# Optimization experiments

Measured on AMD Instinct MI355X. Metric: run time of the kernel, lower is better.

Reference implementation:

```python
import jax, jax.numpy as jnp
import numpy as np

B, D, FD, HW, NH, NC = 8, 384, 256, 64, 8, 4
NP = HW * HW
HD = D // NH


def _ln(x, g, b, eps=1e-5):
    m = jnp.mean(x, -1, keepdims=True)
    v = jnp.mean((x - m) ** 2, -1, keepdims=True)
    return (x - m) / jnp.sqrt(v + eps) * g + b


def _grn(x, g, b, eps=1e-6):
    # x: [B, D, H, W]; global L2 norm per channel over spatial dims
    gx = jnp.sqrt(jnp.sum(x * x, axis=(-2, -1), keepdims=True))  # [B,D,1,1]
    nx = gx / (jnp.mean(gx, axis=-3, keepdims=True) + eps)
    return (1.0 + g[:, None, None]) * (x * nx) + b[:, None, None] + x


def _adaln(x, film, W, bW, g, b):
    gb = film @ W.T + bW                       # [B, 2D]
    gamma, beta = jnp.split(gb, 2, axis=-1)
    return _grn(x, g, b) * (1.0 + gamma)[:, :, None, None] + beta[:, :, None, None]


def setup_inputs() -> dict:
    ks = jax.random.split(jax.random.key(0), 24)
    n = lambda k, s: jax.random.normal(k, s, jnp.float32)
    w = lambda k, o, i: n(k, (o, i)) * 0.02
    return {
        "image": n(ks[0], (B, D, HW, HW)),
        "film_vector": n(ks[1], (B, FD)),
        "perm": jax.random.permutation(ks[2], NP).astype(jnp.int32),
        "Wq": w(ks[3], D, D), "bq": jnp.zeros(D),
        "Wk": w(ks[4], D, D), "bk": jnp.zeros(D),
        "Wv": w(ks[5], D, D), "bv": jnp.zeros(D),
        "Wo": w(ks[6], D, D), "bo": jnp.zeros(D),
        "lnq_g": jnp.ones(D), "lnq_b": jnp.zeros(D),
        "lnk_g": jnp.ones(D), "lnk_b": jnp.zeros(D),
        "ada1_W": n(ks[7], (2 * D, FD)) * 0.001, "ada1_b": jnp.zeros(2 * D),
        "grn1_g": jnp.zeros(D), "grn1_b": jnp.zeros(D),
        "ada2_W": n(ks[8], (2 * D, FD)) * 0.001, "ada2_b": jnp.zeros(2 * D),
        "grn2_g": jnp.zeros(D), "grn2_b": jnp.zeros(D),
        "conv1_W": w(ks[9], 4 * D, D), "conv1_b": jnp.zeros(4 * D),
        "conv2_W": w(ks[10], D, 4 * D), "conv2_b": jnp.zeros(D),
        "cloud_scalar": jnp.ones(D),
        "ffn_scalar": jnp.ones(D),
        "final_scalar": jnp.ones(D) * 0.1,
        "num_clouds": NC,
    }


def reference(image, film_vector, perm, Wq, bq, Wk, bk, Wv, bv, Wo, bo,
              lnq_g, lnq_b, lnk_g, lnk_b, ada1_W, ada1_b, grn1_g, grn1_b,
              ada2_W, ada2_b, grn2_g, grn2_b, conv1_W, conv1_b, conv2_W, conv2_b,
              cloud_scalar, ffn_scalar, final_scalar, num_clouds):
    b, d, h, w = image.shape
    tp = h * w
    gs = tp // num_clouds

    # ---- cloud attention branch ----
    x = _adaln(image, film_vector, ada1_W, ada1_b, grn1_g, grn1_b)
    x_sh = x.reshape(b, d, tp)[:, :, perm]                       # shuffled pixels
    xg = x_sh.transpose(0, 2, 1).reshape(b * num_clouds, gs, d)  # [b*nc, gs, d]

    q = _ln(xg @ Wq.T + bq, lnq_g, lnq_b)
    k = _ln(xg @ Wk.T + bk, lnk_g, lnk_b)
    v = (xg @ Wv.T + bv).reshape(-1, gs, NH, HD)
    q = jax.nn.elu(q.reshape(-1, gs, NH, HD)) + 1.0
    k = jax.nn.elu(k.reshape(-1, gs, NH, HD)) + 1.0

    kv = jnp.einsum('bnhd,bnhe->bhde', k, v)                 # [b*nc, H, hd, hd]
    ksum = k.sum(axis=1)                                      # [b*nc, H, hd]
    num = jnp.einsum('bqhd,bhde->bqhe', q, kv)
    den = jnp.einsum('bqhd,bhd->bqh', q, ksum)[..., None] + 1e-8
    ao = (num / den).reshape(-1, gs, d) @ Wo.T + bo           # [b*nc, gs, d]

    ao = ao.reshape(b, num_clouds, gs, d).transpose(0, 3, 1, 2).reshape(b, d, tp)
    inv_perm = jnp.argsort(perm)
    ao = ao[:, :, inv_perm].reshape(b, d, h, w)

    wi = image + ao * cloud_scalar[:, None, None]

    # ---- FFN branch (1x1 convs) ----
    x2 = _adaln(wi, film_vector, ada2_W, ada2_b, grn2_g, grn2_b)
    h1 = jax.nn.silu(jnp.einsum('bdhw,ed->behw', x2, conv1_W) + conv1_b[:, None, None])
    fo = jnp.einsum('behw,de->bdhw', h1, conv2_W) + conv2_b[:, None, None]
    wi = wi + fo * ffn_scalar[:, None, None]

    return image + wi * final_scalar[:, None, None]
```

## Files before the change

kernel.cpp:

```cpp
#include <hip/hip_runtime.h>
#include <hip/hip_bf16.h>
#include <math.h>

#define BB      8
#define DD      384
#define FDIM    256
#define NPIX    4096
#define NHEAD   8
#define NCLOUD  4
#define HDIM    48
#define GSZ     1024
#define TT      (BB*NPIX)
#define DHID    (4*DD)
#define TD      1152

typedef __hip_bfloat16 bf16;
typedef __attribute__((ext_vector_type(8))) short bf16x8;
typedef __attribute__((ext_vector_type(4))) float f32x4;

__device__ __forceinline__ float b2f(bf16 x){ return __bfloat162float(x); }
__device__ __forceinline__ bf16  f2b(float x){ return __float2bfloat16(x); }
__device__ __forceinline__ float lo2f(unsigned u){ union{unsigned i; float f;} c; c.i = u << 16; return c.f; }
__device__ __forceinline__ float hi2f(unsigned u){ union{unsigned i; float f;} c; c.i = u & 0xffff0000u; return c.f; }
__device__ __forceinline__ unsigned short f2bs(float x){ bf16 b = f2b(x); return *(unsigned short*)&b; }
__device__ __forceinline__ unsigned pack2(float a, float b){
    return (unsigned)f2bs(a) | ((unsigned)f2bs(b) << 16);
}

#if defined(__has_builtin)
#if __has_builtin(__builtin_amdgcn_global_load_lds)
#define USE_GLL 1
#endif
#endif
#ifndef USE_GLL
#define USE_GLL 0
#endif

typedef __attribute__((address_space(1))) void gas_t;
typedef __attribute__((address_space(3))) void las_t;
__device__ __forceinline__ void gload16(const void* g, void* l){
#if USE_GLL
    __builtin_amdgcn_global_load_lds((gas_t*)(void*)g, (las_t*)l, 16, 0, 0);
#else
    *(bf16x8*)l = *(const bf16x8*)g;
#endif
}

__device__ __forceinline__ float block_sum(float v, float* sm, int nthreads){
    #pragma unroll
    for (int o = 32; o > 0; o >>= 1) v += __shfl_down(v, o, 64);
    int nw = nthreads >> 6;
    __syncthreads();
    if ((threadIdx.x & 63) == 0) sm[threadIdx.x >> 6] = v;
    __syncthreads();
    float s = sm[0];
    for (int i = 1; i < nw; i++) s += sm[i];
    return s;
}

#define WSEG 147456
#define WBIG 589824
__global__ void prologue(const float* Wq, const float* Wk, const float* Wv, const float* Wo,
                         const float* W1, const float* W2, bf16* wb,
                         const float* film, const float* ada1_W, const float* ada1_b,
                         const float* ada2_W, const float* ada2_b, float* gb1, float* gb2,
                         const int* perm, int* invp,
                         const float* bq, const float* bk, const float* bv, float* bqkv,
                         float* gxsq, float* gxsq2){
    int blk = blockIdx.x, tid = threadIdx.x;
    if (blk < 6912){
        int i = blk*256 + tid;
        float v;
        if      (i <   WSEG) v = Wq[i];
        else if (i < 2*WSEG) v = Wk[i -   WSEG];
        else if (i < 3*WSEG) v = Wv[i - 2*WSEG];
        else if (i < 4*WSEG) v = Wo[i - 3*WSEG];
        else if (i < 4*WSEG + WBIG) v = W1[i - 4*WSEG];
        else v = W2[i - 4*WSEG - WBIG];
        wb[i] = f2b(v);
    } else if (blk < 6960){
        int idx = (blk-6912)*256 + tid;
        int which = idx / (BB*768);
        int r = idx % (BB*768);
        int bb = r / 768, j = r % 768;
        const float* W = which ? ada2_W : ada1_W;
        const float* bi = which ? ada2_b : ada1_b;
        const float* f = film + bb*FDIM;
        const float* w = W + (size_t)j*FDIM;
        float s = 0.f;
        for (int i = 0; i < FDIM; i++) s += f[i]*w[i];
        (which ? gb2 : gb1)[bb*768 + j] = s + bi[j];
    } else if (blk < 6976){
        int i = (blk-6960)*256 + tid;
        if (i < NPIX) invp[perm[i]] = i;
    } else if (blk < 6981){
        int i = (blk-6976)*256 + tid;
        if (i < 384) bqkv[i] = bq[i];
        else if (i < 768) bqkv[i] = bk[i-384];
        else if (i < 1152) bqkv[i] = bv[i-768];
    } else {
        int i = (blk-6981)*256 + tid;
        if (i < BB*DD){ gxsq[i] = 0.f; gxsq2[i] = 0.f; }
    }
}

__global__ void prep1(const float* img, bf16* imgT, float* gxsq){
    __shared__ float tile[32][33];
    __shared__ float red[32][8];
    int b = blockIdx.z, p0 = blockIdx.x*32, d0 = blockIdx.y*32;
    int tx = threadIdx.x, ty = threadIdx.y;
    #pragma unroll
    for (int i = 0; i < 32; i += 8)
        tile[ty+i][tx] = img[((size_t)b*DD + d0+ty+i)*NPIX + p0+tx];
    __syncthreads();
    #pragma unroll
    for (int i = 0; i < 32; i += 8){
        int p = p0 + ty + i;
        imgT[((size_t)(b<<12) + p)*DD + d0+tx] = f2b(tile[tx][ty+i]);
    }
    float s = 0.f;
    #pragma unroll
    for (int k = 0; k < 4; k++){ float v = tile[tx][ty*4 + k]; s += v*v; }
    red[tx][ty] = s;
    __syncthreads();
    if (ty == 0){
        float t2 = 0.f;
        #pragma unroll
        for (int k = 0; k < 8; k++) t2 += red[tx][k];
        atomicAdd(&gxsq[b*DD + d0+tx], t2);
    }
}

template<bool SQ>
__global__ void grn_nx(const float* gin, float* nx){
    __shared__ float sm[6];
    int b = blockIdx.x; int d = threadIdx.x;
    float g = gin[b*DD + d];
    if (SQ) g = sqrtf(g);
    float tot = block_sum(g, sm, 384);
    nx[b*DD + d] = g / (tot/(float)DD + 1e-6f);
}

__global__ __launch_bounds__(256) void adaln1_tok(const bf16* imgT, const float* nx,
                        const float* gg, const float* gbv, const float* gb,
                        const int* invp, bf16* xt){
    int t = blockIdx.x*4 + (threadIdx.x >> 6);
    int lane = threadIdx.x & 63;
    int b = t >> 12, p = t & 4095;
    int j = invp[p];
    const unsigned* src = (const unsigned*)(imgT + (size_t)t*DD);
    unsigned* dst = (unsigned*)(xt + ((size_t)(b<<12) + j)*DD);
    int d0 = lane*6;
    const float* nxp = nx + b*DD + d0;
    const float* g1 = gb + b*768 + d0;
    const float* g2 = gb + b*768 + 384 + d0;
    #pragma unroll
    for (int i = 0; i < 3; i++){
        unsigned u = src[lane*3 + i];
        float v0 = lo2f(u), v1 = hi2f(u);
        int dd0 = 2*i, dd1 = 2*i+1;
        float r0 = ((1.f + gg[d0+dd0])*(v0*nxp[dd0]) + gbv[d0+dd0] + v0)*(1.f + g1[dd0]) + g2[dd0];
        float r1 = ((1.f + gg[d0+dd1])*(v1*nxp[dd1]) + gbv[d0+dd1] + v1)*(1.f + g1[dd1]) + g2[dd1];
        dst[lane*3 + i] = pack2(r0, r1);
    }
}

__global__ __launch_bounds__(256) void adaln2_tok(const bf16* wi, const float* nx,
                        const float* gg, const float* gbv, const float* gb, bf16* xout){
    int t = blockIdx.x*4 + (threadIdx.x >> 6);
    int lane = threadIdx.x & 63;
    int b = t >> 12;
    const unsigned* src = (const unsigned*)(wi + (size_t)t*DD);
    unsigned* dst = (unsigned*)(xout + (size_t)t*DD);
    int d0 = lane*6;
    const float* nxp = nx + b*DD + d0;
    const float* g1 = gb + b*768 + d0;
    const float* g2 = gb + b*768 + 384 + d0;
    #pragma unroll
    for (int i = 0; i < 3; i++){
        unsigned u = src[lane*3 + i];
        float v0 = lo2f(u), v1 = hi2f(u);
        int dd0 = 2*i, dd1 = 2*i+1;
        float r0 = ((1.f + gg[d0+dd0])*(v0*nxp[dd0]) + gbv[d0+dd0] + v0)*(1.f + g1[dd0]) + g2[dd0];
        float r1 = ((1.f + gg[d0+dd1])*(v1*nxp[dd1]) + gbv[d0+dd1] + v1)*(1.f + g1[dd1]) + g2[dd1];
        dst[lane*3 + i] = pack2(r0, r1);
    }
}

template<int EPI>
__global__ __launch_bounds__(256) void gemm_mfma(const bf16* __restrict__ A,
                          const bf16* __restrict__ W,
                          const float* __restrict__ bias,
                          bf16* __restrict__ C,
                          int M, int N, int K, const int* __restrict__ rowmap){
    __shared__ short lds_[8192];
    int tid  = threadIdx.x;
    int lane = tid & 63, wid = tid >> 6;
    int quad = lane >> 4, l16 = lane & 15;
    int wm = (wid >> 1) * 64, wn = (wid & 1) * 64;

    int v = blockIdx.y * gridDim.x + blockIdx.x;
    int xcd = v & 7, ii = v >> 3;
    int by = xcd * 32 + ii / gridDim.x;
    int bx = ii % gridDim.x;
    int m0 = by * 128, n0 = bx * 128;

    const bf16* sp[4]; short* lp[4];
    #pragma unroll
    for (int it = 0; it < 4; it++){
        int s = tid + it*256;
        int half = s >> 9;
        int r = (s >> 2) & 127;
        int seg = s & 3;
        sp[it] = (half ? W + (size_t)(n0 + r)*K : A + (size_t)(m0 + r)*K) + seg*8;
        lp[it] = lds_ + (size_t)s*8;
    }

    f32x4 acc[4][4] = {};
    for (int k0 = 0; k0 < K; k0 += 32){
        #pragma unroll
        for (int it = 0; it < 4; it++) gload16(sp[it] + k0, lp[it]);
        __syncthreads();
        bf16x8 af[4], wf[4];
        #pragma unroll
        for (int t = 0; t < 4; t++){
            af[t] = *(const bf16x8*)(void*)(lds_ + (wm + t*16 + l16)*32 + quad*8);
            wf[t] = *(const bf16x8*)(void*)(lds_ + 4096 + (wn + t*16 + l16)*32 + quad*8);
        }
        #pragma unroll
        for (int i = 0; i < 4; i++)
            #pragma unroll
            for (int j2 = 0; j2 < 4; j2++)
                acc[i][j2] = __builtin_amdgcn_mfma_f32_16x16x32_bf16(af[i], wf[j2], acc[i][j2], 0, 0, 0);
        __syncthreads();
    }
    int colbase = n0 + wn + l16;
    float bs[4];
    #pragma unroll
    for (int j2 = 0; j2 < 4; j2++) bs[j2] = bias[colbase + j2*16];
    #pragma unroll
    for (int i = 0; i < 4; i++){
        #pragma unroll
        for (int r = 0; r < 4; r++){
            int row = m0 + wm + i*16 + quad*4 + r;
            int grow = rowmap ? ((row & ~4095) | rowmap[row & 4095]) : row;
            bf16* cp = C + (size_t)grow*N + colbase;
            #pragma unroll
            for (int j2 = 0; j2 < 4; j2++){
                float vv = acc[i][j2][r] + bs[j2];
                if (EPI == 1) vv = vv / (1.f + __expf(-vv));
                cp[j2*16] = f2b(vv);
            }
        }
    }
}

__global__ __launch_bounds__(256) void ln_elu_qk(bf16* qkv,
                        const float* gq, const float* bq2,
                        const float* gk, const float* bk2){
    int r = blockIdx.x*4 + (threadIdx.x >> 6);
    int lane = threadIdx.x & 63;
    int t = r >> 1, which = r & 1;
    unsigned* row32 = (unsigned*)(qkv + (size_t)t*TD + which*384);
    const float* g = which ? gk : gq;
    const float* b = which ? bk2 : bq2;
    unsigned u[3];
    #pragma unroll
    for (int i = 0; i < 3; i++) u[i] = row32[lane*3 + i];
    float vv[6];
    #pragma unroll
    for (int i = 0; i < 3; i++){ vv[2*i] = lo2f(u[i]); vv[2*i+1] = hi2f(u[i]); }
    float s = 0.f;
    #pragma unroll
    for (int i = 0; i < 6; i++) s += vv[i];
    #pragma unroll
    for (int o = 32; o > 0; o >>= 1) s += __shfl_xor(s, o, 64);
    float mean = s / (float)DD;
    float s2 = 0.f;
    #pragma unroll
    for (int i = 0; i < 6; i++){ float d = vv[i]-mean; s2 += d*d; }
    #pragma unroll
    for (int o = 32; o > 0; o >>= 1) s2 += __shfl_xor(s2, o, 64);
    float rstd = rsqrtf(s2/(float)DD + 1e-5f);
    int d0 = lane*6;
    #pragma unroll
    for (int i = 0; i < 3; i++){
        float y0 = (vv[2*i]-mean)*rstd*g[d0+2*i] + b[d0+2*i];
        float y1 = (vv[2*i+1]-mean)*rstd*g[d0+2*i+1] + b[d0+2*i+1];
        y0 = (y0 > 0.f) ? y0 : expm1f(y0);
        y1 = (y1 > 0.f) ? y1 : expm1f(y1);
        row32[lane*3 + i] = pack2(y0 + 1.f, y1 + 1.f);
    }
}

__global__ __launch_bounds__(256) void kv_ksum_part(const bf16* qkv, float* kvp, float* ksp){
    int bch = blockIdx.x >> 3, sub = blockIdx.x & 7;
    int bc = bch >> 3, h = bch & 7;
    __shared__ float ks[16][49];
    __shared__ float vs[16][49];
    int eg = (threadIdx.x >> 4) * 3;
    int fg = (threadIdx.x & 15) * 3;
    float acc[3][3] = {};
    float ksacc[3] = {};
    int nbase = bc*GSZ + sub*128;
    for (int n0 = 0; n0 < 128; n0 += 16){
        for (int i = threadIdx.x; i < 16*48; i += 256){
            int n = i/48, e = i%48;
            size_t base = (size_t)(nbase + n0 + n)*TD + h*HDIM;
            ks[n][e] = b2f(qkv[base + 384 + e]);
            vs[n][e] = b2f(qkv[base + 768 + e]);
        }
        __syncthreads();
        #pragma unroll 4
        for (int n = 0; n < 16; n++){
            float ka[3], vb[3];
            #pragma unroll
            for (int i = 0; i < 3; i++){ ka[i] = ks[n][eg+i]; vb[i] = vs[n][fg+i]; }
            #pragma unroll
            for (int i = 0; i < 3; i++)
                #pragma unroll
                for (int j = 0; j < 3; j++)
                    acc[i][j] += ka[i]*vb[j];
            if ((threadIdx.x & 15) == 0){
                #pragma unroll
                for (int i = 0; i < 3; i++) ksacc[i] += ka[i];
            }
        }
        __syncthreads();
    }
    float* kvo = kvp + (size_t)blockIdx.x*2304;
    #pragma unroll
    for (int i = 0; i < 3; i++)
        #pragma unroll
        for (int j = 0; j < 3; j++)
            kvo[(eg+i)*48 + fg+j] = acc[i][j];
    if ((threadIdx.x & 15) == 0){
        #pragma unroll
        for (int i = 0; i < 3; i++) ksp[(size_t)blockIdx.x*48 + eg+i] = ksacc[i];
    }
}

__global__ void kv_reduce(const float* kvp, const float* ksp, float* kv, float* ksum){
    int idx = blockIdx.x*256 + threadIdx.x;
    if (idx < 256*2304){
        int bch = idx / 2304, r = idx - bch*2304;
        const float* p = kvp + (size_t)bch*8*2304 + r;
        float s = 0.f;
        #pragma unroll
        for (int u = 0; u < 8; u++) s += p[u*2304];
        kv[idx] = s;
    } else if (idx < 256*2304 + 256*48){
        int k2 = idx - 256*2304;
        int bch = k2 / 48, r = k2 - bch*48;
        const float* p = ksp + (size_t)bch*8*48 + r;
        float s = 0.f;
        #pragma unroll
        for (int u = 0; u < 8; u++) s += p[u*48];
        ksum[k2] = s;
    }
}

__global__ __launch_bounds__(256) void attn_apply(const bf16* qkv, const float* kv,
                                                  const float* ksum, bf16* out){
    __shared__ float kvs[HDIM*HDIM];
    __shared__ float kss[HDIM];
    __shared__ float qrow[16][HDIM+2];
    __shared__ float dens[16];
    int bch = blockIdx.x >> 2, rs = blockIdx.x & 3;
    int bc = bch >> 3, h = bch & 7;
    const float* kvh = kv + (size_t)bch*HDIM*HDIM;
    for (int i = threadIdx.x; i < HDIM*HDIM; i += 256) kvs[i] = kvh[i];
    if (threadIdx.x < HDIM) kss[threadIdx.x] = ksum[(size_t)bch*HDIM + threadIdx.x];
    __syncthreads();
    int rr = threadIdx.x >> 4;
    int ff = threadIdx.x & 15;
    for (int r0 = rs*256; r0 < rs*256 + 256; r0 += 16){
        for (int i = threadIdx.x; i < 16*HDIM; i += 256){
            int r = i/HDIM, e = i%HDIM;
            qrow[r][e] = b2f(qkv[(size_t)(bc*GSZ + r0 + r)*TD + h*HDIM + e]);
        }
        __syncthreads();
        if (ff == 0){
            float s = 0.f;
            #pragma unroll
            for (int e = 0; e < HDIM; e++) s += qrow[rr][e]*kss[e];
            dens[rr] = s + 1e-8f;
        }
        __syncthreads();
        float inv = 1.f / dens[rr];
        float o0 = 0.f, o1 = 0.f, o2 = 0.f;
        #pragma unroll 8
        for (int e = 0; e < HDIM; e++){
            float qe = qrow[rr][e];
            o0 += qe*kvs[e*HDIM + ff];
            o1 += qe*kvs[e*HDIM + ff + 16];
            o2 += qe*kvs[e*HDIM + ff + 32];
        }
        bf16* orow = out + (size_t)(bc*GSZ + r0 + rr)*DD + h*HDIM;
        orow[ff]      = f2b(o0*inv);
        orow[ff + 16] = f2b(o1*inv);
        orow[ff + 32] = f2b(o2*inv);
        __syncthreads();
    }
}

__global__ __launch_bounds__(256) void build_wi_colsq(const bf16* imgT, const bf16* aot,
                        const float* cs, bf16* wi, float* gxsq2){
    __shared__ float red[4][DD];
    int wave = threadIdx.x >> 6, lane = threadIdx.x & 63;
    int t0 = blockIdx.x*128 + wave*32;
    int b = (blockIdx.x*128) >> 12;
    int d0 = lane*6;
    float c[6];
    #pragma unroll
    for (int i = 0; i < 6; i++) c[i] = cs[d0+i];
    float acc[6] = {};
    for (int it = 0; it < 32; it++){
        size_t t = (size_t)(t0 + it);
        const unsigned* pi = (const unsigned*)(imgT + t*DD);
        const unsigned* pa = (const unsigned*)(aot + t*DD);
        unsigned* pw = (unsigned*)(wi + t*DD);
        #pragma unroll
        for (int i = 0; i < 3; i++){
            unsigned ui = pi[lane*3 + i];
            unsigned ua = pa[lane*3 + i];
            float v0 = lo2f(ui) + lo2f(ua)*c[2*i];
            float v1 = hi2f(ui) + hi2f(ua)*c[2*i+1];
            acc[2*i]   += v0*v0;
            acc[2*i+1] += v1*v1;
            pw[lane*3 + i] = pack2(v0, v1);
        }
    }
    #pragma unroll
    for (int i = 0; i < 6; i++) red[wave][d0+i] = acc[i];
    __syncthreads();
    for (int d = threadIdx.x; d < DD; d += 256){
        float s = red[0][d] + red[1][d] + red[2][d] + red[3][d];
        atomicAdd(&gxsq2[b*DD + d], s);
    }
}

__global__ void final_out(const float* img, const bf16* wi, const bf16* fot,
                          const float* ffs, const float* fins, float* out){
    __shared__ float tile[32][33];
    int b = blockIdx.z, p0 = blockIdx.x*32, d0 = blockIdx.y*32;
    int tx = threadIdx.x, ty = threadIdx.y;
    #pragma unroll
    for (int i = 0; i < 32; i += 8){
        size_t t = (size_t)(b<<12) + p0+ty+i;
        tile[ty+i][tx] = b2f(wi[t*DD + d0+tx]) + b2f(fot[t*DD + d0+tx])*ffs[d0+tx];
    }
    __syncthreads();
    #pragma unroll
    for (int i = 0; i < 32; i += 8){
        int d = d0 + ty + i;
        size_t o = ((size_t)b*DD + d)*NPIX + p0+tx;
        out[o] = img[o] + tile[tx][ty+i]*fins[d];
    }
}

extern "C" void kernel_launch(void* const* d_in, const int* in_sizes, int n_in,
                              void* d_out, int out_size, void* d_ws, size_t ws_size,
                              hipStream_t stream){
    const float* image   = (const float*)d_in[0];
    const float* film    = (const float*)d_in[1];
    const int*   perm    = (const int*)  d_in[2];
    const float* Wq      = (const float*)d_in[3];
    const float* bq      = (const float*)d_in[4];
    const float* Wk      = (const float*)d_in[5];
    const float* bk      = (const float*)d_in[6];
    const float* Wv      = (const float*)d_in[7];
    const float* bv      = (const float*)d_in[8];
    const float* Wo      = (const float*)d_in[9];
    const float* bo      = (const float*)d_in[10];
    const float* lnq_g   = (const float*)d_in[11];
    const float* lnq_b   = (const float*)d_in[12];
    const float* lnk_g   = (const float*)d_in[13];
    const float* lnk_b   = (const float*)d_in[14];
    const float* ada1_W  = (const float*)d_in[15];
    const float* ada1_b  = (const float*)d_in[16];
    const float* grn1_g  = (const float*)d_in[17];
    const float* grn1_b  = (const float*)d_in[18];
    const float* ada2_W  = (const float*)d_in[19];
    const float* ada2_b  = (const float*)d_in[20];
    const float* grn2_g  = (const float*)d_in[21];
    const float* grn2_b  = (const float*)d_in[22];
    const float* conv1_W = (const float*)d_in[23];
    const float* conv1_b = (const float*)d_in[24];
    const float* conv2_W = (const float*)d_in[25];
    const float* conv2_b = (const float*)d_in[26];
    const float* cs      = (const float*)d_in[27];
    const float* ffs     = (const float*)d_in[28];
    const float* fins    = (const float*)d_in[29];
    float* out = (float*)d_out;

    char* m = (char*)d_ws;
    float* gb1     = (float*)m;  m += (size_t)BB*768*4;
    float* gb2     = (float*)m;  m += (size_t)BB*768*4;
    int*   invp    = (int*)m;    m += (size_t)NPIX*4;
    float* gxsq    = (float*)m;  m += (size_t)BB*DD*4;
    float* gxsq2   = (float*)m;  m += (size_t)BB*DD*4;
    float* nx      = (float*)m;  m += (size_t)BB*DD*4;
    float* kvbuf   = (float*)m;  m += (size_t)256*HDIM*HDIM*4;
    float* ksumbuf = (float*)m;  m += (size_t)256*HDIM*4;
    float* kvp     = (float*)m;  m += (size_t)2048*2304*4;
    float* ksp     = (float*)m;  m += (size_t)2048*48*4;
    float* bqkv    = (float*)m;  m += (size_t)TD*4;
    bf16*  wb      = (bf16*)m;   m += (size_t)(4*WSEG + 2*WBIG)*2;
    bf16*  wqkv = wb;
    bf16*  wbo  = wb + 3*WSEG;
    bf16*  wb1  = wb + 4*WSEG, *wb2 = wb + 4*WSEG + WBIG;
    bf16* imgT = (bf16*)m;       m += (size_t)TT*DD*2;
    bf16* qkv = (bf16*)m;        m += (size_t)TT*TD*2;
    bf16* obf = (bf16*)m;        m += (size_t)TT*DD*2;
    bf16* abf = (bf16*)m;        m += (size_t)TT*DD*2;
    bf16* wi  = (bf16*)m;        m += (size_t)TT*DD*2;
    bf16* H1  = qkv;

    prologue<<<6993, 256, 0, stream>>>(Wq, Wk, Wv, Wo, conv1_W, conv2_W, wb,
                                       film, ada1_W, ada1_b, ada2_W, ada2_b, gb1, gb2,
                                       perm, invp, bq, bk, bv, bqkv, gxsq, gxsq2);

    prep1<<<dim3(128,12,BB), dim3(32,8), 0, stream>>>(image, imgT, gxsq);
    grn_nx<true><<<BB, DD, 0, stream>>>(gxsq, nx);
    adaln1_tok<<<TT/4, 256, 0, stream>>>(imgT, nx, grn1_g, grn1_b, gb1, invp, abf);
    gemm_mfma<0><<<dim3(9,256), 256, 0, stream>>>(abf, wqkv, bqkv, qkv, TT, TD, DD, nullptr);
    ln_elu_qk<<<2*TT/4, 256, 0, stream>>>(qkv, lnq_g, lnq_b, lnk_g, lnk_b);
    kv_ksum_part<<<2048, 256, 0, stream>>>(qkv, kvp, ksp);
    kv_reduce<<<2352, 256, 0, stream>>>(kvp, ksp, kvbuf, ksumbuf);
    attn_apply<<<1024, 256, 0, stream>>>(qkv, kvbuf, ksumbuf, abf);
    gemm_mfma<0><<<dim3(3,256), 256, 0, stream>>>(abf, wbo, bo, obf, TT, DD, DD, perm);
    build_wi_colsq<<<BB*32, 256, 0, stream>>>(imgT, obf, cs, wi, gxsq2);

    grn_nx<true><<<BB, DD, 0, stream>>>(gxsq2, nx);
    adaln2_tok<<<TT/4, 256, 0, stream>>>(wi, nx, grn2_g, grn2_b, gb2, abf);
    gemm_mfma<1><<<dim3(12,256), 256, 0, stream>>>(abf, wb1, conv1_b, H1, TT, DHID, DD, nullptr);
    gemm_mfma<0><<<dim3(3,256), 256, 0, stream>>>(H1, wb2, conv2_b, abf, TT, DD, DHID, nullptr);
    final_out<<<dim3(128,12,BB), dim3(32,8), 0, stream>>>(image, wi, abf, ffs, fins, out);
}
```

Baseline: 603.8 us.

## Compute linear-attention apply with bf16 MFMA, folding denominator into augmented matrix

Replaces the scalar FP32 shared-memory loop in attn_apply with bf16 MFMA 16x16x32 instructions. The kv matrix and ksum are packed into a zero-padded 64x64 bf16 operand, so the denominator comes out as an extra output column and is broadcast with a shuffle. This removes the per-16-row sync loop and the scalar FMAs, and reads Q with vector loads directly from global memory. The cost is bf16 rounding of kv and ksum, including in the denominator, which may change accuracy.

```diff
diff --git a/kernel.cpp b/kernel.cpp
--- a/kernel.cpp
+++ b/kernel.cpp
@@ -360,47 +360,58 @@
     }
 }
 
-__global__ __launch_bounds__(256) void attn_apply(const bf16* qkv, const float* kv,
-                                                  const float* ksum, bf16* out){
-    __shared__ float kvs[HDIM*HDIM];
-    __shared__ float kss[HDIM];
-    __shared__ float qrow[16][HDIM+2];
-    __shared__ float dens[16];
+__global__ __launch_bounds__(256) void attn_apply(const bf16* __restrict__ qkv,
+                                                  const float* __restrict__ kv,
+                                                  const float* __restrict__ ksum,
+                                                  bf16* __restrict__ out){
+    __shared__ __align__(16) bf16 Wm[64][72];
     int bch = blockIdx.x >> 2, rs = blockIdx.x & 3;
     int bc = bch >> 3, h = bch & 7;
-    const float* kvh = kv + (size_t)bch*HDIM*HDIM;
-    for (int i = threadIdx.x; i < HDIM*HDIM; i += 256) kvs[i] = kvh[i];
-    if (threadIdx.x < HDIM) kss[threadIdx.x] = ksum[(size_t)bch*HDIM + threadIdx.x];
-    __syncthreads();
-    int rr = threadIdx.x >> 4;
-    int ff = threadIdx.x & 15;
-    for (int r0 = rs*256; r0 < rs*256 + 256; r0 += 16){
-        for (int i = threadIdx.x; i < 16*HDIM; i += 256){
-            int r = i/HDIM, e = i%HDIM;
-            qrow[r][e] = b2f(qkv[(size_t)(bc*GSZ + r0 + r)*TD + h*HDIM + e]);
-        }
-        __syncthreads();
-        if (ff == 0){
-            float s = 0.f;
-            #pragma unroll
-            for (int e = 0; e < HDIM; e++) s += qrow[rr][e]*kss[e];
-            dens[rr] = s + 1e-8f;
-        }
-        __syncthreads();
-        float inv = 1.f / dens[rr];
-        float o0 = 0.f, o1 = 0.f, o2 = 0.f;
-        #pragma unroll 8
-        for (int e = 0; e < HDIM; e++){
-            float qe = qrow[rr][e];
-            o0 += qe*kvs[e*HDIM + ff];
-            o1 += qe*kvs[e*HDIM + ff + 16];
-            o2 += qe*kvs[e*HDIM + ff + 32];
-        }
-        bf16* orow = out + (size_t)(bc*GSZ + r0 + rr)*DD + h*HDIM;
-        orow[ff]      = f2b(o0*inv);
-        orow[ff + 16] = f2b(o1*inv);
-        orow[ff + 32] = f2b(o2*inv);
-        __syncthreads();
+    int tid = threadIdx.x;
+    int lane = tid & 63, w = tid >> 6;
+    int l16 = lane & 15, quad = lane >> 4;
+
+    for (int i = tid; i < 64*72; i += 256) ((unsigned short*)Wm)[i] = 0;
+    __syncthreads();
+    const float* kvh = kv + (size_t)bch*(HDIM*HDIM);
+    for (int i = tid; i < HDIM*HDIM; i += 256){
+        int e = i / HDIM, f = i - e*HDIM;
+        Wm[f][e] = f2b(kvh[i]);
+    }
+    if (tid < HDIM) Wm[HDIM][tid] = f2b(ksum[(size_t)bch*HDIM + tid]);
+    __syncthreads();
+
+    bf16x8 bw[4][2];
+    #pragma unroll
+    for (int n = 0; n < 4; n++){
+        bw[n][0] = *(const bf16x8*)(void*)&Wm[n*16 + l16][quad*8];
+        bw[n][1] = *(const bf16x8*)(void*)&Wm[n*16 + l16][32 + quad*8];
+    }
+
+    int rowbase0 = bc*GSZ + rs*256 + w*64;
+    #pragma unroll
+    for (int frag = 0; frag < 4; frag++){
+        int arow = rowbase0 + frag*16 + l16;
+        const bf16* qp = qkv + (size_t)arow*TD + h*HDIM;
+        bf16x8 a0 = *(const bf16x8*)(void*)(qp + quad*8);
+        bf16x8 a1 = {};
+        if (quad < 2) a1 = *(const bf16x8*)(void*)(qp + 32 + quad*8);
+        f32x4 acc[4] = {};
+        #pragma unroll
+        for (int n = 0; n < 4; n++){
+            acc[n] = __builtin_amdgcn_mfma_f32_16x16x32_bf16(a0, bw[n][0], acc[n], 0, 0, 0);
+            acc[n] = __builtin_amdgcn_mfma_f32_16x16x32_bf16(a1, bw[n][1], acc[n], 0, 0, 0);
+        }
+        int orow0 = rowbase0 + frag*16 + quad*4;
+        #pragma unroll
+        for (int r = 0; r < 4; r++){
+            float den = __shfl(acc[3][r], quad*16, 64);
+            float inv = 1.f / (den + 1e-8f);
+            bf16* op = out + (size_t)(orow0 + r)*DD + h*HDIM + l16;
+            op[0]  = f2b(acc[0][r]*inv);
+            op[16] = f2b(acc[1][r]*inv);
+            op[32] = f2b(acc[2][r]*inv);
+        }
     }
 }
 
```

Result: faster. 548.2 us (-9.2%).
